# Kernel optimization log

Hardware: AMD Instinct MI355X
Metric: run time of the kernel (lower is better)

## Reference

```python
import jax, jax.numpy as jnp
import numpy as np

B, CIN, COUT, H, W = 16, 128, 128, 64, 64
K1, K2, DIL = 3, 3, 1
PAD0 = DIL * (K1 - 1) // 2
PAD1 = DIL * (K2 - 1) // 2
L = H * W


def setup_inputs() -> dict:
    key = jax.random.key(0)
    k1, k2, k3, k4, k5 = jax.random.split(key, 5)
    x = jax.random.normal(k1, (B, CIN, H, W), dtype=jnp.float32)
    # binary per-pixel mask over kernel taps, broadcast over batch*channels
    mask = (jax.random.uniform(k2, (1, K1 * K2, L)) < 0.5).astype(jnp.float32)
    fan_in = CIN * K1 * K2
    bound = 1.0 / np.sqrt(fan_in)
    weight = jax.random.uniform(k3, (COUT, CIN, K1, K2), jnp.float32, -bound, bound)
    mask_weight = jax.random.uniform(k4, (COUT, K1, K2), jnp.float32, -bound, bound)
    bias = jax.random.uniform(k5, (COUT,), jnp.float32, -bound, bound)
    return {"x": x, "mask": mask, "weight": weight, "mask_weight": mask_weight, "bias": bias}


def reference(x, mask, weight, mask_weight, bias):
    # im2col: [B, CIN*K1*K2, H, W]; channel ordering (cin, k1, k2) matches torch unfold
    patches = jax.lax.conv_general_dilated_patches(
        x, (K1, K2), (1, 1), [(PAD0, PAD0), (PAD1, PAD1)], rhs_dilation=(DIL, DIL))
    p = patches.reshape(B, CIN, K1 * K2, L)
    p = p * mask[:, None, :, :]          # mask [1, K, L] broadcasts over B and CIN
    p = p.reshape(B, CIN * K1 * K2, L)
    out = jnp.einsum('ok,bkl->bol', weight.reshape(COUT, -1), p)
    out = out + bias[None, :, None]
    out = out + jnp.einsum('ok,mkl->mol', mask_weight.reshape(COUT, -1), mask)
    return out.reshape(B, COUT, H, W)
```

## Files before the change

kernel.cpp:

```cpp
#include <hip/hip_runtime.h>
#include <stdint.h>

#define B_    16
#define CIN_  128
#define COUT_ 128
#define H_    64
#define W_    64
#define L_    4096
#define KK_   1152

typedef unsigned short u16;
typedef __bf16 bf16x8 __attribute__((ext_vector_type(8)));
typedef float  floatx4 __attribute__((ext_vector_type(4)));
typedef uint32_t u32x4 __attribute__((ext_vector_type(4)));

typedef const __attribute__((address_space(1))) uint32_t* gptr_t;
typedef __attribute__((address_space(3))) uint32_t*       lptr_t;

__device__ __forceinline__ void async_copy16(const void* g, void* l) {
    __builtin_amdgcn_global_load_lds((gptr_t)g, (lptr_t)l, 16, 0, 0);
}

__device__ __forceinline__ u16 f2bf(float f) {
    uint32_t u = __builtin_bit_cast(uint32_t, f);
    uint32_t r = u + 0x7FFFu + ((u >> 16) & 1u);
    return (u16)(r >> 16);
}

__global__ void lmc_prep_kernel(const float* __restrict__ mask, const float* __restrict__ mw,
                                const float* __restrict__ bias, const float* __restrict__ w,
                                float* __restrict__ mb, u16* __restrict__ wb2) {
    const int bid = blockIdx.x, tid = threadIdx.x;
    if (bid < 128) {
        const int o = bid;
        float m[9];
        #pragma unroll
        for (int k = 0; k < 9; ++k) m[k] = mw[o * 9 + k];
        const float bs = bias[o];
        for (int l = tid; l < L_; l += 256) {
            float s = bs;
            #pragma unroll
            for (int k = 0; k < 9; ++k) s += m[k] * mask[k * L_ + l];
            mb[o * L_ + l] = s;
        }
    } else {
        const int base = (bid - 128) * 2304;
        #pragma unroll
        for (int i = 0; i < 9; ++i) {
            const int e = base + i * 256 + tid;
            const int k = e >> 14;
            const int rem = e & 16383;
            const int o = rem >> 7, c = rem & 127;
            wb2[e] = f2bf(w[(size_t)o * KK_ + c * 9 + k]);
        }
    }
}

__global__ __launch_bounds__(512, 2)
void lmc_gemm_kernel(const float* __restrict__ x, const u16* __restrict__ wb2,
                     const float* __restrict__ mask, const float* __restrict__ mb,
                     float* __restrict__ out) {
    __shared__ u16 W_lds[384 * 128];
    __shared__ u16 A_lds[2][128 * 128];

    const int flat    = blockIdx.x;
    const int logical = (flat & 7) * 32 + (flat >> 3);
    const int b       = logical >> 4;
    const int lt      = logical & 15;
    const int Y       = lt * 4;
    const int l0      = lt * 256;

    const int tid  = threadIdx.x;
    const int lane = tid & 63;
    const int wv   = tid >> 6;
    const int wm   = (wv >> 2) * 64;
    const int wn   = (wv & 3) * 64;
    const int lrow = lane & 15;
    const int quad = lane >> 4;

    {
        const int cg    = lane >> 4;
        const int x0    = (lane & 15) * 4;
        const int cbase = wv * 16 + cg * 4;
        const int d     = wv * 2 + (cg >> 1);
        const int half8 = (cg & 1) * 8;
        const float* xc = x + ((size_t)(b * CIN_ + cbase) * L_) + x0;

        #pragma unroll
        for (int wy = 0; wy < 6; ++wy) {
            const int y   = Y - 1 + wy;
            const int px0 = wy * 64 + x0;
            if (y >= 0 && y <= 63) {
                const float* xr = xc + y * 64;
                float4 v0 = *reinterpret_cast<const float4*>(xr);
                float4 v1 = *reinterpret_cast<const float4*>(xr + L_);
                float4 v2 = *reinterpret_cast<const float4*>(xr + 2 * L_);
                float4 v3 = *reinterpret_cast<const float4*>(xr + 3 * L_);
                const float* p0 = (const float*)&v0;
                const float* p1 = (const float*)&v1;
                const float* p2 = (const float*)&v2;
                const float* p3 = (const float*)&v3;
                #pragma unroll
                for (int j = 0; j < 4; ++j) {
                    const int px   = px0 + j;
                    const int slot = d ^ (px & 7);
                    uint2 pk;
                    pk.x = (uint32_t)f2bf(p0[j]) | ((uint32_t)f2bf(p1[j]) << 16);
                    pk.y = (uint32_t)f2bf(p2[j]) | ((uint32_t)f2bf(p3[j]) << 16);
                    *reinterpret_cast<uint2*>((char*)W_lds + px * 256 + slot * 16 + half8) = pk;
                }
            } else {
                const uint2 z2 = {0u, 0u};
                #pragma unroll
                for (int j = 0; j < 4; ++j) {
                    const int px   = px0 + j;
                    const int slot = d ^ (px & 7);
                    *reinterpret_cast<uint2*>((char*)W_lds + px * 256 + slot * 16 + half8) = z2;
                }
            }
        }
    }

    const char* wb2_c = (const char*)wb2;
    char* A_c = (char*)A_lds;
    uint32_t aoff[4];
    #pragma unroll
    for (int ti = 0; ti < 4; ++ti) {
        const int r  = 16 * wv + 4 * ti + (lane >> 4);
        const int sc = (lane & 15) ^ (r & 7);
        aoff[ti] = (uint32_t)(r * 256 + sc * 16);
    }
    #pragma unroll
    for (int ti = 0; ti < 4; ++ti)
        async_copy16(wb2_c + aoff[ti], A_c + (wv * 4 + ti) * 1024);

    int pix0[4];
    uint64_t bits = 0;
    #pragma unroll
    for (int j = 0; j < 4; ++j) {
        const int ll = wn + j * 16 + lrow;
        const int xx = ll & 63;
        pix0[j] = ((ll >> 6) + 1) * 64 + xx;
        const int lg = l0 + ll;
        #pragma unroll
        for (int k = 0; k < 9; ++k) {
            const int dx  = k % 3 - 1;
            const bool ok = (xx + dx >= 0) && (xx + dx < 64) &&
                            (mask[k * L_ + lg] != 0.0f);
            if (ok) bits |= (1ull << (k * 4 + j));
        }
    }

    floatx4 acc[4][4];
    #pragma unroll
    for (int i = 0; i < 4; ++i)
        #pragma unroll
        for (int j = 0; j < 4; ++j)
            acc[i][j] = (floatx4){0.f, 0.f, 0.f, 0.f};

    asm volatile("s_waitcnt vmcnt(0) lgkmcnt(0)" ::: "memory");
    __builtin_amdgcn_s_barrier();
    asm volatile("" ::: "memory");

    for (int k = 0; k < 9; ++k) {
        if (k < 8) {
            const int koff = (k + 1) * 32768;
            char* dstb = A_c + ((k + 1) & 1) * 32768;
            #pragma unroll
            for (int ti = 0; ti < 4; ++ti)
                async_copy16(wb2_c + koff + aoff[ti], dstb + (wv * 4 + ti) * 1024);
        }

        const int dy = k / 3 - 1;
        const int dx = k - (k / 3) * 3 - 1;
        const int sh = dy * 64 + dx;

        uint32_t kp[4];
        #pragma unroll
        for (int j = 0; j < 4; ++j)
            kp[j] = 0u - (uint32_t)((bits >> (k * 4 + j)) & 1ull);

        const u16* Ac = (const u16*)(A_c + (k & 1) * 32768);

        #pragma unroll
        for (int ks = 0; ks < 4; ++ks) {
            bf16x8 af[4], bf[4];
            #pragma unroll
            for (int i = 0; i < 4; ++i) {
                const int orow = wm + i * 16 + lrow;
                const int slot = (ks * 4 + quad) ^ (orow & 7);
                af[i] = *reinterpret_cast<const bf16x8*>(&Ac[orow * 128 + slot * 8]);
            }
            #pragma unroll
            for (int j = 0; j < 4; ++j) {
                int p = pix0[j] + sh;
                p = (p < 0) ? 0 : p;
                p = (p > 383) ? 383 : p;
                const int slot = (ks * 4 + quad) ^ (p & 7);
                bf16x8 v = *reinterpret_cast<const bf16x8*>(&W_lds[p * 128 + slot * 8]);
                u32x4 t = __builtin_bit_cast(u32x4, v);
                t &= kp[j];
                bf[j] = __builtin_bit_cast(bf16x8, t);
            }
            __builtin_amdgcn_s_setprio(1);
            #pragma unroll
            for (int i = 0; i < 4; ++i)
                #pragma unroll
                for (int j = 0; j < 4; ++j)
                    acc[i][j] = __builtin_amdgcn_mfma_f32_16x16x32_bf16(
                        af[i], bf[j], acc[i][j], 0, 0, 0);
            __builtin_amdgcn_s_setprio(0);
        }

        if (k < 8) {
            asm volatile("s_waitcnt vmcnt(0)" ::: "memory");
            __builtin_amdgcn_s_barrier();
            asm volatile("" ::: "memory");
        }
    }

    #pragma unroll
    for (int i = 0; i < 4; ++i) {
        #pragma unroll
        for (int j = 0; j < 4; ++j) {
            const int l = l0 + wn + j * 16 + lrow;
            #pragma unroll
            for (int r = 0; r < 4; ++r) {
                const int o = wm + i * 16 + quad * 4 + r;
                out[((size_t)b * COUT_ + o) * L_ + l] = acc[i][j][r] + mb[o * L_ + l];
            }
        }
    }
}

extern "C" void kernel_launch(void* const* d_in, const int* in_sizes, int n_in,
                              void* d_out, int out_size, void* d_ws, size_t ws_size,
                              hipStream_t stream) {
    const float* x      = (const float*)d_in[0];
    const float* mask   = (const float*)d_in[1];
    const float* weight = (const float*)d_in[2];
    const float* mw     = (const float*)d_in[3];
    const float* bias   = (const float*)d_in[4];
    float* out = (float*)d_out;

    char* ws = (char*)d_ws;
    u16*   wb2 = (u16*)ws;
    float* mb  = (float*)(ws + 294912);

    lmc_prep_kernel<<<192, 256, 0, stream>>>(mask, mw, bias, weight, mb, wb2);
    lmc_gemm_kernel<<<256, 512, 0, stream>>>(x, wb2, mask, mb, out);
}
```

Baseline: 117.4 us.

## Software-pipeline LDS fragment loads one k-step ahead of MFMAs with ping-pong registers

Restructures the main loop so LDS reads for the next k-substep go into a second register set while the MFMAs for the current substep run. Workgroup barriers and explicit waitcnts are inserted around each phase to keep warps in lockstep, in the style of a ping-pong schedule. The intent is to hide LDS read latency behind matrix work. In exchange it adds two barriers per substep, roughly 72 in total, and uses more registers for the doubled fragment sets, which may hurt occupancy or add stall time.

```diff
diff --git a/kernel.cpp b/kernel.cpp
--- a/kernel.cpp
+++ b/kernel.cpp
@@ -55,6 +55,62 @@
         }
     }
 }
+
+#define PHASE(CUR, NXT, kk, ks)                                                \
+    do {                                                                       \
+        if ((ks) == 0 && (kk) < 8) {                                           \
+            const int koff_ = ((kk) + 1) * 32768;                              \
+            char* dstb_ = A_c + (((kk) + 1) & 1) * 32768;                      \
+            _Pragma("unroll")                                                  \
+            for (int ti = 0; ti < 4; ++ti)                                     \
+                async_copy16(wb2_c + koff_ + aoff[ti],                         \
+                             dstb_ + (wv * 4 + ti) * 1024);                    \
+        }                                                                      \
+        if ((kk) * 4 + (ks) < 35) {                                            \
+            const int kn_  = ((ks) < 3) ? (kk) : (kk) + 1;                     \
+            const int ksn_ = ((ks) < 3) ? (ks) + 1 : 0;                        \
+            const u16* An_ = (const u16*)(A_c + (kn_ & 1) * 32768);            \
+            const int shn_ = (kn_ / 3 - 1) * 64 + (kn_ % 3) - 1;               \
+            _Pragma("unroll")                                                  \
+            for (int i = 0; i < 4; ++i) {                                      \
+                const int orow = wm + i * 16 + lrow;                           \
+                const int slot = (ksn_ * 4 + quad) ^ (orow & 7);               \
+                NXT##a[i] = *reinterpret_cast<const bf16x8*>(                  \
+                    &An_[orow * 128 + slot * 8]);                              \
+            }                                                                  \
+            _Pragma("unroll")                                                  \
+            for (int j = 0; j < 4; ++j) {                                      \
+                int p = pix0[j] + shn_;                                        \
+                p = (p < 0) ? 0 : (p > 383 ? 383 : p);                         \
+                const int slot = (ksn_ * 4 + quad) ^ (p & 7);                  \
+                NXT##b[j] = *reinterpret_cast<const bf16x8*>(                  \
+                    &W_lds[p * 128 + slot * 8]);                               \
+            }                                                                  \
+        }                                                                      \
+        if ((ks) == 2)                                                         \
+            asm volatile("s_waitcnt vmcnt(0)" ::: "memory");                   \
+        __builtin_amdgcn_s_barrier();                                          \
+        asm volatile("s_waitcnt lgkmcnt(0)" ::: "memory");                     \
+        __builtin_amdgcn_sched_barrier(0);                                     \
+        {                                                                      \
+            bf16x8 bm[4];                                                      \
+            _Pragma("unroll")                                                  \
+            for (int j = 0; j < 4; ++j) {                                      \
+                u32x4 t = __builtin_bit_cast(u32x4, CUR##b[j]);                \
+                t &= (0u - (uint32_t)((bits >> ((kk) * 4 + j)) & 1ull));       \
+                bm[j] = __builtin_bit_cast(bf16x8, t);                         \
+            }                                                                  \
+            __builtin_amdgcn_s_setprio(1);                                     \
+            _Pragma("unroll")                                                  \
+            for (int i = 0; i < 4; ++i)                                        \
+                _Pragma("unroll")                                              \
+                for (int j = 0; j < 4; ++j)                                    \
+                    acc[i][j] = __builtin_amdgcn_mfma_f32_16x16x32_bf16(       \
+                        CUR##a[i], bm[j], acc[i][j], 0, 0, 0);                 \
+            __builtin_amdgcn_s_setprio(0);                                     \
+        }                                                                      \
+        __builtin_amdgcn_s_barrier();                                          \
+    } while (0)
 
 __global__ __launch_bounds__(512, 2)
 void lmc_gemm_kernel(const float* __restrict__ x, const u16* __restrict__ wb2,
@@ -162,61 +218,30 @@
     __builtin_amdgcn_s_barrier();
     asm volatile("" ::: "memory");
 
+    bf16x8 S0a[4], S0b[4], S1a[4], S1b[4];
+    {
+        const u16* A0 = (const u16*)A_c;
+        #pragma unroll
+        for (int i = 0; i < 4; ++i) {
+            const int orow = wm + i * 16 + lrow;
+            const int slot = quad ^ (orow & 7);
+            S0a[i] = *reinterpret_cast<const bf16x8*>(&A0[orow * 128 + slot * 8]);
+        }
+        const int sh0 = -65;
+        #pragma unroll
+        for (int j = 0; j < 4; ++j) {
+            int p = pix0[j] + sh0;
+            p = (p < 0) ? 0 : p;
+            const int slot = quad ^ (p & 7);
+            S0b[j] = *reinterpret_cast<const bf16x8*>(&W_lds[p * 128 + slot * 8]);
+        }
+    }
+
     for (int k = 0; k < 9; ++k) {
-        if (k < 8) {
-            const int koff = (k + 1) * 32768;
-            char* dstb = A_c + ((k + 1) & 1) * 32768;
-            #pragma unroll
-            for (int ti = 0; ti < 4; ++ti)
-                async_copy16(wb2_c + koff + aoff[ti], dstb + (wv * 4 + ti) * 1024);
-        }
-
-        const int dy = k / 3 - 1;
-        const int dx = k - (k / 3) * 3 - 1;
-        const int sh = dy * 64 + dx;
-
-        uint32_t kp[4];
-        #pragma unroll
-        for (int j = 0; j < 4; ++j)
-            kp[j] = 0u - (uint32_t)((bits >> (k * 4 + j)) & 1ull);
-
-        const u16* Ac = (const u16*)(A_c + (k & 1) * 32768);
-
-        #pragma unroll
-        for (int ks = 0; ks < 4; ++ks) {
-            bf16x8 af[4], bf[4];
-            #pragma unroll
-            for (int i = 0; i < 4; ++i) {
-                const int orow = wm + i * 16 + lrow;
-                const int slot = (ks * 4 + quad) ^ (orow & 7);
-                af[i] = *reinterpret_cast<const bf16x8*>(&Ac[orow * 128 + slot * 8]);
-            }
-            #pragma unroll
-            for (int j = 0; j < 4; ++j) {
-                int p = pix0[j] + sh;
-                p = (p < 0) ? 0 : p;
-                p = (p > 383) ? 383 : p;
-                const int slot = (ks * 4 + quad) ^ (p & 7);
-                bf16x8 v = *reinterpret_cast<const bf16x8*>(&W_lds[p * 128 + slot * 8]);
-                u32x4 t = __builtin_bit_cast(u32x4, v);
-                t &= kp[j];
-                bf[j] = __builtin_bit_cast(bf16x8, t);
-            }
-            __builtin_amdgcn_s_setprio(1);
-            #pragma unroll
-            for (int i = 0; i < 4; ++i)
-                #pragma unroll
-                for (int j = 0; j < 4; ++j)
-                    acc[i][j] = __builtin_amdgcn_mfma_f32_16x16x32_bf16(
-                        af[i], bf[j], acc[i][j], 0, 0, 0);
-            __builtin_amdgcn_s_setprio(0);
-        }
-
-        if (k < 8) {
-            asm volatile("s_waitcnt vmcnt(0)" ::: "memory");
-            __builtin_amdgcn_s_barrier();
-            asm volatile("" ::: "memory");
-        }
+        PHASE(S0, S1, k, 0);
+        PHASE(S1, S0, k, 1);
+        PHASE(S0, S1, k, 2);
+        PHASE(S1, S0, k, 3);
     }
 
     #pragma unroll
```

Result: slower. 124.5 us (+6.1%).
